# Performance work log

Measured on AMD Instinct MI355X. Metric: run time of the kernel, lower is better.

Reference implementation:

```python
import jax, jax.numpy as jnp
import numpy as np

NA, NF, EA, EF, NG = 200000, 50000, 800000, 200000, 4096
D = 128
BN_EPS = 1e-5

def _bn(x, g, b):
    m = x.mean(axis=0)
    v = x.var(axis=0)
    return g * (x - m) * jax.lax.rsqrt(v + BN_EPS) + b

def _gine(x, src, dst, edge_emb, W1, b1, g1, be1, W2, b2):
    # message = relu(x_src + edge_emb); scatter-add to dst; (1+eps)*x with eps=0
    msg = jax.nn.relu(x[src] + edge_emb)
    agg = jax.ops.segment_sum(msg, dst, num_segments=x.shape[0])
    h = x + agg
    h = jax.nn.relu(_bn(h @ W1 + b1, g1, be1))
    return h @ W2 + b2

def _seg_mean(x, idx, n):
    s = jax.ops.segment_sum(x, idx, num_segments=n)
    c = jax.ops.segment_sum(jnp.ones((x.shape[0],), x.dtype), idx, num_segments=n)
    return s / jnp.maximum(c, 1.0)[:, None]

def setup_inputs() -> dict:
    key = jax.random.key(0)
    ks = jax.random.split(key, 40)
    def nrm(i, shape, scale=0.05):
        return (jax.random.normal(ks[i], shape, dtype=jnp.float32) * scale)
    inp = {
        'atom_x': jax.random.normal(ks[0], (NA, 101), dtype=jnp.float32),
        'fg_x': jax.random.normal(ks[1], (NF, 73), dtype=jnp.float32),
        'atom_edge_attr': jax.random.normal(ks[2], (EA, 11), dtype=jnp.float32),
        'fg_edge_attr': jax.random.normal(ks[3], (EF, 101), dtype=jnp.float32),
        'atom_emb_W': nrm(4, (101, D)), 'atom_emb_b': jnp.zeros((D,), jnp.float32),
        'fg_emb_W': nrm(5, (73, D)), 'fg_emb_b': jnp.zeros((D,), jnp.float32),
        'bond_W': nrm(6, (3, 11, D)), 'bond_b': jnp.zeros((3, D), jnp.float32),
        'ag_W1': nrm(7, (3, D, 2 * D)), 'ag_b1': jnp.zeros((3, 2 * D), jnp.float32),
        'ag_g1': jnp.ones((3, 2 * D), jnp.float32), 'ag_be1': jnp.zeros((3, 2 * D), jnp.float32),
        'ag_W2': nrm(8, (3, 2 * D, D)), 'ag_b2': jnp.zeros((3, D), jnp.float32),
        'abn_g': jnp.ones((3, D), jnp.float32), 'abn_b': jnp.zeros((3, D), jnp.float32),
        'fge_W': nrm(9, (2, 101, D)), 'fge_b': jnp.zeros((2, D), jnp.float32),
        'fg_W1': nrm(10, (2, D, 2 * D)), 'fg_b1': jnp.zeros((2, 2 * D), jnp.float32),
        'fg_g1': jnp.ones((2, 2 * D), jnp.float32), 'fg_be1': jnp.zeros((2, 2 * D), jnp.float32),
        'fg_W2': nrm(11, (2, 2 * D, D)), 'fg_b2': jnp.zeros((2, D), jnp.float32),
        'fbn_g': jnp.ones((2, D), jnp.float32), 'fbn_b': jnp.zeros((2, D), jnp.float32),
        'a2f_W': nrm(12, (D, D)), 'a2f_b': jnp.zeros((D,), jnp.float32),
        'atom_edge_index': jax.random.randint(ks[13], (2, EA), 0, NA, dtype=jnp.int32),
        'fg_edge_index': jax.random.randint(ks[14], (2, EF), 0, NF, dtype=jnp.int32),
        'atom_idx': jax.random.randint(ks[15], (NA,), 0, NA, dtype=jnp.int32),
        'fg_idx': jax.random.randint(ks[16], (NA,), 0, NF, dtype=jnp.int32),
        'fg_batch': jnp.sort(jax.random.randint(ks[17], (NF,), 0, NG, dtype=jnp.int32)),
    }
    return inp

def reference(atom_x, fg_x, atom_edge_attr, fg_edge_attr, atom_emb_W, atom_emb_b, fg_emb_W, fg_emb_b, bond_W, bond_b, ag_W1, ag_b1, ag_g1, ag_be1, ag_W2, ag_b2, abn_g, abn_b, fge_W, fge_b, fg_W1, fg_b1, fg_g1, fg_be1, fg_W2, fg_b2, fbn_g, fbn_b, a2f_W, a2f_b, atom_edge_index, fg_edge_index, atom_idx, fg_idx, fg_batch):
    asrc, adst = atom_edge_index[0], atom_edge_index[1]
    fsrc, fdst = fg_edge_index[0], fg_edge_index[1]
    h = atom_x @ atom_emb_W + atom_emb_b
    for i in range(3):
        eemb = atom_edge_attr @ bond_W[i] + bond_b[i]
        h = _gine(h, asrc, adst, eemb, ag_W1[i], ag_b1[i], ag_g1[i], ag_be1[i], ag_W2[i], ag_b2[i])
        h = _bn(h, abn_g[i], abn_b[i])
        if i != 2:
            h = jax.nn.relu(h)
    a2f = _seg_mean(h[atom_idx], fg_idx, NF) @ a2f_W + a2f_b
    g = fg_x @ fg_emb_W + fg_emb_b + a2f
    for i in range(2):
        eemb = fg_edge_attr @ fge_W[i] + fge_b[i]
        g = _gine(g, fsrc, fdst, eemb, fg_W1[i], fg_b1[i], fg_g1[i], fg_be1[i], fg_W2[i], fg_b2[i])
        g = _bn(g, fbn_g[i], fbn_b[i])
        if i != 1:
            g = jax.nn.relu(g)
    return _seg_mean(g, fg_batch, NG)
```

## Files before the change

### kernel.cpp

```cpp
#include <hip/hip_runtime.h>
#include <cstddef>
#include <cstdint>

#define NA_C 200000
#define NF_C 50000
#define EA_C 800000
#define EF_C 200000
#define NG_C 4096
#define DD 128
#define HH 256
#define SC_CHUNK 2048

typedef unsigned short u16;
typedef unsigned int   u32;
typedef float f32x4 __attribute__((ext_vector_type(4)));
typedef short s16x8 __attribute__((ext_vector_type(8)));

__device__ inline float bf2f(u16 h) { return __uint_as_float(((u32)h) << 16); }
__device__ inline u16 f2bf(float f) {
    u32 u = __float_as_uint(f);
    return (u16)((u + 0x7fffu + ((u >> 16) & 1u)) >> 16);
}
__device__ inline float2 up2(u32 u) {
    return make_float2(__uint_as_float(u << 16), __uint_as_float(u & 0xffff0000u));
}
__device__ inline u32 pk2(float x, float y) { return (u32)f2bf(x) | ((u32)f2bf(y) << 16); }

__global__ __launch_bounds__(256) void gemm_b(
    const u16* __restrict__ A, const u16* __restrict__ Bt,
    const float* __restrict__ bias,
    const float* __restrict__ iscale, const float* __restrict__ ishift,
    const u16* __restrict__ Cadd, u16* __restrict__ C,
    int M, int K, int Ntot,
    float* __restrict__ ssum, float* __restrict__ ssq)
{
    __shared__ u16 As[4 * 128 * 8];
    __shared__ u16 Bs[4 * 128 * 8];
    __shared__ float ls[128], lq[128];
    const int tid  = threadIdx.x;
    const int wave = tid >> 6, lane = tid & 63;
    const int quad = lane >> 4, l15 = lane & 15;
    const int wm = (wave & 1) * 64, wn = (wave >> 1) * 64;
    const int m0 = blockIdx.y * 128, n0 = blockIdx.x * 128;
    const int r     = tid >> 1;
    const int cpair = (tid & 1) * 2;

    f32x4 acc[4][4];
#pragma unroll
    for (int i = 0; i < 4; ++i)
#pragma unroll
        for (int j = 0; j < 4; ++j) acc[i][j] = (f32x4)0.f;

    const int m = m0 + r;
    for (int k0 = 0; k0 < K; k0 += 32) {
#pragma unroll
        for (int j = 0; j < 2; ++j) {
            const int cg = cpair + j;
            uint4 av = make_uint4(0, 0, 0, 0);
            if (m < M) av = *(const uint4*)(A + (size_t)m * K + k0 + cg * 8);
            if (iscale) {
                u32* w = (u32*)&av;
#pragma unroll
                for (int q2 = 0; q2 < 4; ++q2) {
                    int kk = k0 + cg * 8 + q2 * 2;
                    float2 f = up2(w[q2]);
                    f.x = fmaxf(fmaf(f.x, iscale[kk],     ishift[kk]),     0.f);
                    f.y = fmaxf(fmaf(f.y, iscale[kk + 1], ishift[kk + 1]), 0.f);
                    w[q2] = pk2(f.x, f.y);
                }
            }
            *(uint4*)&As[(cg * 128 + r) * 8] = av;
        }
#pragma unroll
        for (int j = 0; j < 2; ++j) {
            const int cg = cpair + j;
            uint4 bv = *(const uint4*)(Bt + (size_t)(n0 + r) * K + k0 + cg * 8);
            *(uint4*)&Bs[(cg * 128 + r) * 8] = bv;
        }
        __syncthreads();

        s16x8 a[4], b[4];
#pragma unroll
        for (int mi = 0; mi < 4; ++mi)
            a[mi] = *(const s16x8*)&As[(quad * 128 + wm + mi * 16 + l15) * 8];
#pragma unroll
        for (int ni = 0; ni < 4; ++ni)
            b[ni] = *(const s16x8*)&Bs[(quad * 128 + wn + ni * 16 + l15) * 8];
#pragma unroll
        for (int mi = 0; mi < 4; ++mi)
#pragma unroll
            for (int ni = 0; ni < 4; ++ni)
                acc[mi][ni] = __builtin_amdgcn_mfma_f32_16x16x32_bf16(
                    a[mi], b[ni], acc[mi][ni], 0, 0, 0);
        __syncthreads();
    }

    if (ssum) {
        if (tid < 128) { ls[tid] = 0.f; lq[tid] = 0.f; }
        __syncthreads();
    }

    float cs[4] = {0.f, 0.f, 0.f, 0.f}, cq[4] = {0.f, 0.f, 0.f, 0.f};
#pragma unroll
    for (int mi = 0; mi < 4; ++mi) {
        int rowb = m0 + wm + mi * 16 + quad * 4;
#pragma unroll
        for (int ni = 0; ni < 4; ++ni) {
            int col = n0 + wn + ni * 16 + l15;
            float bv = bias[col];
#pragma unroll
            for (int rr = 0; rr < 4; ++rr) {
                int row = rowb + rr;
                if (row < M) {
                    float v = acc[mi][ni][rr] + bv;
                    size_t idx = (size_t)row * Ntot + col;
                    if (Cadd) v += bf2f(Cadd[idx]);
                    C[idx] = f2bf(v);
                    cs[ni] += v;
                    cq[ni] = fmaf(v, v, cq[ni]);
                }
            }
        }
    }

    if (ssum) {
#pragma unroll
        for (int ni = 0; ni < 4; ++ni) {
            int lc = wn + ni * 16 + l15;
            atomicAdd(&ls[lc], cs[ni]);
            atomicAdd(&lq[lc], cq[ni]);
        }
        __syncthreads();
        if (tid < 128) {
            atomicAdd(&ssum[n0 + tid], ls[tid]);
            atomicAdd(&ssq[n0 + tid], lq[tid]);
        }
    }
}

static inline void gemm_launch(hipStream_t s, const u16* A, const u16* Bt,
    const float* bias, const float* iscale, const float* ishift,
    const u16* Cadd, u16* C, int M, int K, int Ntot,
    float* ssum = nullptr, float* ssq = nullptr)
{
    dim3 grid(Ntot / 128, (M + 127) / 128);
    gemm_b<<<grid, dim3(256), 0, s>>>(A, Bt, bias, iscale, ishift, Cadd, C,
                                      M, K, Ntot, ssum, ssq);
}

__global__ void cvt_pad(const float* __restrict__ src, u32* __restrict__ dst,
                        int M, int K, int Kp2)
{
    int idx = blockIdx.x * 256 + threadIdx.x;
    if (idx >= M * Kp2) return;
    int row = idx / Kp2, c = (idx - row * Kp2) * 2;
    float a = (c < K)     ? src[(size_t)row * K + c]     : 0.f;
    float b = (c + 1 < K) ? src[(size_t)row * K + c + 1] : 0.f;
    dst[idx] = pk2(a, b);
}

__global__ void cvt_pad_perm(const float* __restrict__ src, const int2* __restrict__ csr2,
                             u32* __restrict__ dst, int M, int K, int Kp2)
{
    int idx = blockIdx.x * 256 + threadIdx.x;
    if (idx >= M * Kp2) return;
    int row = idx / Kp2, c = (idx - row * Kp2) * 2;
    int srow = csr2[row].x;
    float a = (c < K)     ? src[(size_t)srow * K + c]     : 0.f;
    float b = (c + 1 < K) ? src[(size_t)srow * K + c + 1] : 0.f;
    dst[idx] = pk2(a, b);
}

__global__ void perm_attr12_k(const float* __restrict__ attr, const int2* __restrict__ csr2,
                              float* __restrict__ out, int ne)
{
    int idx = blockIdx.x * 256 + threadIdx.x;
    if (idx >= ne * 12) return;
    int e = idx / 12, k = idx - e * 12;
    int eid = csr2[e].x;
    out[idx] = (k < 11) ? attr[(size_t)eid * 11 + k] : 0.f;
}

__global__ void prep_wt(const float* __restrict__ W, u16* __restrict__ Wt,
                        int K, int N, int Kp)
{
    int idx = blockIdx.x * 256 + threadIdx.x;
    if (idx >= N * Kp) return;
    int n = idx / Kp, k = idx - n * Kp;
    Wt[idx] = (k < K) ? f2bf(W[(size_t)k * N + n]) : (u16)0;
}

__global__ void hist_k(const int* __restrict__ idx, int n, int* __restrict__ deg)
{
    int i = blockIdx.x * 256 + threadIdx.x;
    if (i < n) atomicAdd(&deg[idx[i]], 1);
}

__global__ __launch_bounds__(256) void scan_part_k(const int* __restrict__ deg, int n,
                                                   int* __restrict__ bsum)
{
    __shared__ int ts[256];
    const int t = threadIdx.x;
    const int base = blockIdx.x * SC_CHUNK + t * 8;
    int s = 0;
#pragma unroll
    for (int j = 0; j < 8; ++j) { int i = base + j; if (i < n) s += deg[i]; }
    ts[t] = s;
    __syncthreads();
    for (int off = 128; off > 0; off >>= 1) {
        if (t < off) ts[t] += ts[t + off];
        __syncthreads();
    }
    if (t == 0) bsum[blockIdx.x] = ts[0];
}

__global__ __launch_bounds__(256) void scan_top_k(int* __restrict__ bsum, int nb)
{
    __shared__ int ss[256];
    const int t = threadIdx.x;
    int v = (t < nb) ? bsum[t] : 0;
    ss[t] = v;
    __syncthreads();
    for (int off = 1; off < 256; off <<= 1) {
        int u = (t >= off) ? ss[t - off] : 0;
        __syncthreads();
        ss[t] += u;
        __syncthreads();
    }
    if (t < nb) bsum[t] = ss[t] - v;
}

__global__ __launch_bounds__(256) void scan_emit_k(const int* __restrict__ deg, int n,
                                                   const int* __restrict__ bsum,
                                                   int* __restrict__ rowptr)
{
    __shared__ int ts[256];
    const int t = threadIdx.x;
    const int base = blockIdx.x * SC_CHUNK + t * 8;
    int d[8], loc[8], s = 0;
#pragma unroll
    for (int j = 0; j < 8; ++j) {
        int i = base + j;
        d[j] = (i < n) ? deg[i] : 0;
        loc[j] = s;
        s += d[j];
    }
    ts[t] = s;
    __syncthreads();
    for (int off = 1; off < 256; off <<= 1) {
        int u = (t >= off) ? ts[t - off] : 0;
        __syncthreads();
        ts[t] += u;
        __syncthreads();
    }
    const int off0 = bsum[blockIdx.x] + (ts[t] - s);
#pragma unroll
    for (int j = 0; j < 8; ++j) {
        int i = base + j;
        if (i < n) {
            rowptr[i] = off0 + loc[j];
            if (i == n - 1) rowptr[n] = off0 + loc[j] + d[j];
        }
    }
}

static void csr_prefix(hipStream_t s, const int* idx, int ne, int nbkt,
                       int* rowptr, int* cursor, int* bsum)
{
    hipMemsetAsync(cursor, 0, (size_t)nbkt * 4, s);
    hist_k<<<(ne + 255) / 256, 256, 0, s>>>(idx, ne, cursor);
    int nblk = (nbkt + SC_CHUNK - 1) / SC_CHUNK;
    scan_part_k<<<nblk, 256, 0, s>>>(cursor, nbkt, bsum);
    scan_top_k<<<1, 256, 0, s>>>(bsum, nblk);
    scan_emit_k<<<nblk, 256, 0, s>>>(cursor, nbkt, bsum, rowptr);
    hipMemcpyAsync(cursor, rowptr, (size_t)nbkt * 4, hipMemcpyDeviceToDevice, s);
}

__global__ void fill2_k(const int* __restrict__ idx, const int* __restrict__ src,
                        int n, int* __restrict__ cursor, int2* __restrict__ csr2)
{
    int i = blockIdx.x * 256 + threadIdx.x;
    if (i < n) {
        int p = atomicAdd(&cursor[idx[i]], 1);
        csr2[p] = make_int2(i, src[i]);
    }
}

__global__ void fillm_k(const int* __restrict__ idx, const int* __restrict__ map,
                        int n, int* __restrict__ cursor, int* __restrict__ csr)
{
    int i = blockIdx.x * 256 + threadIdx.x;
    if (i < n) {
        int p = atomicAdd(&cursor[idx[i]], 1);
        csr[p] = map ? map[i] : i;
    }
}

__global__ __launch_bounds__(256, 4) void gine_agg_atom_b(
    const u32* __restrict__ x2, const float4* __restrict__ attrp,
    const int2* __restrict__ csr2, const int* __restrict__ rowptr,
    const float* __restrict__ Wm, const float* __restrict__ bm,
    const float* __restrict__ tsc, const float* __restrict__ tsh, int trelu,
    u32* __restrict__ out2, int n)
{
    const int lane = threadIdx.x & 63;
    const int v = blockIdx.x * 4 + (threadIdx.x >> 6);
    if (v >= n) return;
    float wx[11], wy[11];
#pragma unroll
    for (int k = 0; k < 11; ++k) {
        float2 w = *(const float2*)&Wm[k * 128 + 2 * lane];
        wx[k] = w.x; wy[k] = w.y;
    }
    const float2 bb = *(const float2*)&bm[2 * lane];
    float sc0 = 1.f, sc1 = 1.f, sh0 = 0.f, sh1 = 0.f;
    if (tsc) {
        sc0 = tsc[2 * lane]; sc1 = tsc[2 * lane + 1];
        sh0 = tsh[2 * lane]; sh1 = tsh[2 * lane + 1];
    }
    float2 xv = up2(x2[(size_t)v * 64 + lane]);
    xv.x = fmaf(xv.x, sc0, sh0); xv.y = fmaf(xv.y, sc1, sh1);
    if (trelu) { xv.x = fmaxf(xv.x, 0.f); xv.y = fmaxf(xv.y, 0.f); }
    float2 acc = xv;
    const int e0 = rowptr[v], e1 = rowptr[v + 1];
    if (e0 < e1) {
        int2 pc = csr2[e0];
        int2 pn = csr2[(e0 + 1 < e1) ? e0 + 1 : e0];
        float4 a0c = attrp[3 * (size_t)e0];
        float4 a1c = attrp[3 * (size_t)e0 + 1];
        float4 a2c = attrp[3 * (size_t)e0 + 2];
        u32 xc = x2[(size_t)pc.y * 64 + lane];
        for (int e = e0; e < e1; ++e) {
            const int en  = (e + 1 < e1) ? e + 1 : e;
            const int en2 = (e + 2 < e1) ? e + 2 : en;
            int2 p2 = csr2[en2];
            u32 xn = x2[(size_t)pn.y * 64 + lane];
            float4 a0n = attrp[3 * (size_t)en];
            float4 a1n = attrp[3 * (size_t)en + 1];
            float4 a2n = attrp[3 * (size_t)en + 2];
            float ar[12];
            *(float4*)&ar[0] = a0c; *(float4*)&ar[4] = a1c; *(float4*)&ar[8] = a2c;
            float m0 = bb.x, m1 = bb.y;
#pragma unroll
            for (int k = 0; k < 11; ++k) {
                m0 = fmaf(ar[k], wx[k], m0);
                m1 = fmaf(ar[k], wy[k], m1);
            }
            float2 s = up2(xc);
            s.x = fmaf(s.x, sc0, sh0); s.y = fmaf(s.y, sc1, sh1);
            if (trelu) { s.x = fmaxf(s.x, 0.f); s.y = fmaxf(s.y, 0.f); }
            acc.x += fmaxf(s.x + m0, 0.f);
            acc.y += fmaxf(s.y + m1, 0.f);
            pn = p2; xc = xn;
            a0c = a0n; a1c = a1n; a2c = a2n;
        }
    }
    out2[(size_t)v * 64 + lane] = pk2(acc.x, acc.y);
}

__global__ __launch_bounds__(256) void gine_agg_pre_b(
    const u32* __restrict__ x2, const u32* __restrict__ eemb2,
    const int2* __restrict__ csr2, const int* __restrict__ rowptr,
    const float* __restrict__ tsc, const float* __restrict__ tsh, int trelu,
    u32* __restrict__ out2, int n)
{
    const int lane = threadIdx.x & 63;
    const int v = blockIdx.x * 4 + (threadIdx.x >> 6);
    if (v >= n) return;
    float sc0 = 1.f, sc1 = 1.f, sh0 = 0.f, sh1 = 0.f;
    if (tsc) {
        sc0 = tsc[2 * lane]; sc1 = tsc[2 * lane + 1];
        sh0 = tsh[2 * lane]; sh1 = tsh[2 * lane + 1];
    }
    float2 xv = up2(x2[(size_t)v * 64 + lane]);
    xv.x = fmaf(xv.x, sc0, sh0); xv.y = fmaf(xv.y, sc1, sh1);
    if (trelu) { xv.x = fmaxf(xv.x, 0.f); xv.y = fmaxf(xv.y, 0.f); }
    float2 acc = xv;
    const int e0 = rowptr[v], e1 = rowptr[v + 1];
    if (e0 < e1) {
        int2 pc = csr2[e0];
        int2 pn = csr2[(e0 + 1 < e1) ? e0 + 1 : e0];
        u32  xc = x2[(size_t)pc.y * 64 + lane];
        u32  mc = eemb2[(size_t)e0 * 64 + lane];
        for (int e = e0; e < e1; ++e) {
            const int en  = (e + 1 < e1) ? e + 1 : e;
            const int en2 = (e + 2 < e1) ? e + 2 : en;
            int2 p2 = csr2[en2];
            u32  xn = x2[(size_t)pn.y * 64 + lane];
            u32  mn = eemb2[(size_t)en * 64 + lane];
            float2 m = up2(mc);
            float2 s = up2(xc);
            s.x = fmaf(s.x, sc0, sh0); s.y = fmaf(s.y, sc1, sh1);
            if (trelu) { s.x = fmaxf(s.x, 0.f); s.y = fmaxf(s.y, 0.f); }
            acc.x += fmaxf(m.x + s.x, 0.f);
            acc.y += fmaxf(m.y + s.y, 0.f);
            pn = p2; xc = xn; mc = mn;
        }
    }
    out2[(size_t)v * 64 + lane] = pk2(acc.x, acc.y);
}

__global__ __launch_bounds__(256) void seg_mean_b2b(
    const u32* __restrict__ x2, const int* __restrict__ csr,
    const int* __restrict__ rowptr,
    const float* __restrict__ tsc, const float* __restrict__ tsh,
    u32* __restrict__ out2, int n)
{
    const int lane = threadIdx.x & 63;
    const int v = blockIdx.x * 4 + (threadIdx.x >> 6);
    if (v >= n) return;
    const int e0 = rowptr[v], e1 = rowptr[v + 1];
    float2 acc = make_float2(0.f, 0.f);
    if (e0 < e1) {
        int cc = csr[e0];
        int cn = csr[(e0 + 1 < e1) ? e0 + 1 : e0];
        u32 xc = x2[(size_t)cc * 64 + lane];
        for (int e = e0; e < e1; ++e) {
            const int en  = (e + 1 < e1) ? e + 1 : e;
            const int en2 = (e + 2 < e1) ? e + 2 : en;
            int c2 = csr[en2];
            u32 xn = x2[(size_t)cn * 64 + lane];
            float2 s = up2(xc);
            acc.x += s.x; acc.y += s.y;
            cn = c2; xc = xn;
        }
    }
    float inv = 1.f / fmaxf((float)(e1 - e0), 1.f);
    float2 r = make_float2(acc.x * inv, acc.y * inv);
    if (tsc) {
        if (e1 > e0) {
            r.x = fmaf(r.x, tsc[2 * lane],     tsh[2 * lane]);
            r.y = fmaf(r.y, tsc[2 * lane + 1], tsh[2 * lane + 1]);
        } else {
            r.x = 0.f; r.y = 0.f;
        }
    }
    out2[(size_t)v * 64 + lane] = pk2(r.x, r.y);
}

__global__ __launch_bounds__(256) void seg_mean_b2f(
    const u32* __restrict__ x2, const int* __restrict__ csr,
    const int* __restrict__ rowptr,
    const float* __restrict__ tsc, const float* __restrict__ tsh,
    float* __restrict__ out, int n)
{
    const int lane = threadIdx.x & 63;
    const int v = blockIdx.x * 4 + (threadIdx.x >> 6);
    if (v >= n) return;
    const int e0 = rowptr[v], e1 = rowptr[v + 1];
    float2 acc = make_float2(0.f, 0.f);
    if (e0 < e1) {
        int cc = csr[e0];
        int cn = csr[(e0 + 1 < e1) ? e0 + 1 : e0];
        u32 xc = x2[(size_t)cc * 64 + lane];
        for (int e = e0; e < e1; ++e) {
            const int en  = (e + 1 < e1) ? e + 1 : e;
            const int en2 = (e + 2 < e1) ? e + 2 : en;
            int c2 = csr[en2];
            u32 xn = x2[(size_t)cn * 64 + lane];
            float2 s = up2(xc);
            acc.x += s.x; acc.y += s.y;
            cn = c2; xc = xn;
        }
    }
    float inv = 1.f / fmaxf((float)(e1 - e0), 1.f);
    float2 r = make_float2(acc.x * inv, acc.y * inv);
    if (tsc) {
        if (e1 > e0) {
            r.x = fmaf(r.x, tsc[2 * lane],     tsh[2 * lane]);
            r.y = fmaf(r.y, tsc[2 * lane + 1], tsh[2 * lane + 1]);
        } else {
            r.x = 0.f; r.y = 0.f;
        }
    }
    *(float2*)&out[(size_t)v * 128 + lane * 2] = r;
}

__global__ void bn_finalize(const float* __restrict__ sum, const float* __restrict__ sumsq,
                            const float* __restrict__ g, const float* __restrict__ be,
                            float minv, float* __restrict__ sc, float* __restrict__ sh, int N)
{
    int c = threadIdx.x;
    if (c < N) {
        float m = sum[c] * minv;
        float v = fmaxf(sumsq[c] * minv - m * m, 0.f);
        float s = g[c] * rsqrtf(v + 1e-5f);
        sc[c] = s;
        sh[c] = fmaf(-m, s, be[c]);
    }
}

extern "C" void kernel_launch(void* const* d_in, const int* in_sizes, int n_in,
                              void* d_out, int out_size, void* d_ws, size_t ws_size,
                              hipStream_t stream)
{
    const float* atom_x        = (const float*)d_in[0];
    const float* fg_x          = (const float*)d_in[1];
    const float* atom_edge_attr= (const float*)d_in[2];
    const float* fg_edge_attr  = (const float*)d_in[3];
    const float* atom_emb_W    = (const float*)d_in[4];
    const float* atom_emb_b    = (const float*)d_in[5];
    const float* fg_emb_W      = (const float*)d_in[6];
    const float* fg_emb_b      = (const float*)d_in[7];
    const float* bond_W        = (const float*)d_in[8];
    const float* bond_b        = (const float*)d_in[9];
    const float* ag_W1         = (const float*)d_in[10];
    const float* ag_b1         = (const float*)d_in[11];
    const float* ag_g1         = (const float*)d_in[12];
    const float* ag_be1        = (const float*)d_in[13];
    const float* ag_W2         = (const float*)d_in[14];
    const float* ag_b2         = (const float*)d_in[15];
    const float* abn_g         = (const float*)d_in[16];
    const float* abn_b         = (const float*)d_in[17];
    const float* fge_W         = (const float*)d_in[18];
    const float* fge_b         = (const float*)d_in[19];
    const float* fg_W1         = (const float*)d_in[20];
    const float* fg_b1         = (const float*)d_in[21];
    const float* fg_g1         = (const float*)d_in[22];
    const float* fg_be1        = (const float*)d_in[23];
    const float* fg_W2         = (const float*)d_in[24];
    const float* fg_b2         = (const float*)d_in[25];
    const float* fbn_g         = (const float*)d_in[26];
    const float* fbn_b         = (const float*)d_in[27];
    const float* a2f_W         = (const float*)d_in[28];
    const float* a2f_b         = (const float*)d_in[29];
    const int*   aei           = (const int*)d_in[30];
    const int*   fei           = (const int*)d_in[31];
    const int*   atom_idx      = (const int*)d_in[32];
    const int*   fg_idx        = (const int*)d_in[33];
    const int*   fg_batch      = (const int*)d_in[34];
    const int *asrc = aei, *adst = aei + EA_C;
    const int *fsrc = fei, *fdst = fei + EF_C;

    char* base = (char*)d_ws;
    const size_t SZ_H = (size_t)NA_C * DD * 2;
    u16* hA = (u16*)base;
    u16* hB = (u16*)(base + SZ_H);
    u16* TB = (u16*)(base + 2 * SZ_H);
    u16* XB = (u16*)(base + 2 * SZ_H + (size_t)NA_C * HH * 2);
    char* csrb = (char*)XB + SZ_H;
    int*  aR  = (int*)csrb;
    int*  aCu = aR + (NA_C + 2);
    int*  bS  = aCu + NA_C;
    int2* aE2 = (int2*)(bS + 258);
    char* wtb = (char*)(aE2 + EA_C);
    wtb = (char*)(((uintptr_t)wtb + 15) & ~(uintptr_t)15);
    u16* WT_aemb = (u16*)wtb;                 wtb += 128 * 128 * 2;
    u16* WT_aW1  = (u16*)wtb;                 wtb += 3 * 256 * 128 * 2;
    u16* WT_aW2  = (u16*)wtb;                 wtb += 3 * 128 * 256 * 2;
    u16* WT_a2f  = (u16*)wtb;                 wtb += 128 * 128 * 2;
    u16* WT_femb = (u16*)wtb;                 wtb += 128 * 96 * 2;
    u16* WT_fge  = (u16*)wtb;                 wtb += 2 * 128 * 128 * 2;
    u16* WT_fW1  = (u16*)wtb;                 wtb += 2 * 256 * 128 * 2;
    u16* WT_fW2  = (u16*)wtb;                 wtb += 2 * 128 * 256 * 2;
    float* stats = (float*)wtb;               wtb += 10240 * sizeof(float);
    float* S_SUM = stats;
    float* S_SQ  = stats + 2560;
    float* S_SC  = stats + 5120;
    float* S_SH  = stats + 7680;

    {
        int g = (128 * 128 + 255) / 256;
        prep_wt<<<g, 256, 0, stream>>>(atom_emb_W, WT_aemb, 101, 128, 128);
        prep_wt<<<g, 256, 0, stream>>>(a2f_W, WT_a2f, 128, 128, 128);
        for (int i = 0; i < 3; ++i) {
            prep_wt<<<(256 * 128 + 255) / 256, 256, 0, stream>>>(
                ag_W1 + (size_t)i * 128 * 256, WT_aW1 + (size_t)i * 256 * 128, 128, 256, 128);
            prep_wt<<<(128 * 256 + 255) / 256, 256, 0, stream>>>(
                ag_W2 + (size_t)i * 256 * 128, WT_aW2 + (size_t)i * 128 * 256, 256, 128, 256);
        }
        prep_wt<<<(128 * 96 + 255) / 256, 256, 0, stream>>>(fg_emb_W, WT_femb, 73, 128, 96);
        for (int i = 0; i < 2; ++i) {
            prep_wt<<<g, 256, 0, stream>>>(
                fge_W + (size_t)i * 101 * 128, WT_fge + (size_t)i * 128 * 128, 101, 128, 128);
            prep_wt<<<(256 * 128 + 255) / 256, 256, 0, stream>>>(
                fg_W1 + (size_t)i * 128 * 256, WT_fW1 + (size_t)i * 256 * 128, 128, 256, 128);
            prep_wt<<<(128 * 256 + 255) / 256, 256, 0, stream>>>(
                fg_W2 + (size_t)i * 256 * 128, WT_fW2 + (size_t)i * 128 * 256, 256, 128, 256);
        }
    }
    hipMemsetAsync(stats, 0, 5120 * sizeof(float), stream);

    csr_prefix(stream, adst, EA_C, NA_C, aR, aCu, bS);
    fill2_k<<<(EA_C + 255) / 256, 256, 0, stream>>>(adst, asrc, EA_C, aCu, aE2);

    cvt_pad<<<((size_t)NA_C * 64 + 255) / 256, 256, 0, stream>>>(atom_x, (u32*)XB, NA_C, 101, 64);

    gemm_launch(stream, XB, WT_aemb, atom_emb_b, nullptr, nullptr, nullptr, hA, NA_C, 128, 128);

    float* attrP = (float*)XB;
    perm_attr12_k<<<((size_t)EA_C * 12 + 255) / 256, 256, 0, stream>>>(
        atom_edge_attr, aE2, attrP, EA_C);

    u16* hc = hA;
    const float* cur_sc = nullptr;
    const float* cur_sh = nullptr;
    int cur_relu = 0;
    for (int i = 0; i < 3; ++i) {
        u16* hn = (hc == hA) ? hB : hA;
        const int st1 = 2 * i, st2 = 2 * i + 1;
        gine_agg_atom_b<<<(NA_C + 3) / 4, 256, 0, stream>>>(
            (const u32*)hc, (const float4*)attrP, aE2, aR,
            bond_W + (size_t)i * 11 * DD, bond_b + i * DD,
            cur_sc, cur_sh, cur_relu, (u32*)hn, NA_C);
        gemm_launch(stream, hn, WT_aW1 + (size_t)i * 256 * 128,
                    ag_b1 + i * HH, nullptr, nullptr, nullptr, TB, NA_C, 128, HH,
                    S_SUM + st1 * 256, S_SQ + st1 * 256);
        bn_finalize<<<1, HH, 0, stream>>>(S_SUM + st1 * 256, S_SQ + st1 * 256,
                                          ag_g1 + i * HH, ag_be1 + i * HH,
                                          1.f / NA_C, S_SC + st1 * 256, S_SH + st1 * 256, HH);
        gemm_launch(stream, TB, WT_aW2 + (size_t)i * 128 * 256,
                    ag_b2 + i * DD, S_SC + st1 * 256, S_SH + st1 * 256, nullptr, hn,
                    NA_C, 256, 128,
                    S_SUM + st2 * 256, S_SQ + st2 * 256);
        bn_finalize<<<1, DD, 0, stream>>>(S_SUM + st2 * 256, S_SQ + st2 * 256,
                                          abn_g + i * DD, abn_b + i * DD,
                                          1.f / NA_C, S_SC + st2 * 256, S_SH + st2 * 256, DD);
        cur_sc = S_SC + st2 * 256; cur_sh = S_SH + st2 * 256; cur_relu = (i != 2);
        hc = hn;
    }

    {
        int* xE = (int*)aE2;
        csr_prefix(stream, fg_idx, NA_C, NF_C, aR, aCu, bS);
        fillm_k<<<(NA_C + 255) / 256, 256, 0, stream>>>(fg_idx, atom_idx, NA_C, aCu, xE);
        seg_mean_b2b<<<(NF_C + 3) / 4, 256, 0, stream>>>(
            (const u32*)hc, xE, aR, cur_sc, cur_sh, (u32*)hA, NF_C);
    }
    u16* means   = hA;
    u16* a2f_lin = hA + (size_t)NF_C * DD;
    gemm_launch(stream, means, WT_a2f, a2f_b, nullptr, nullptr, nullptr, a2f_lin, NF_C, 128, 128);

    u16* fgx_bf = hA + (size_t)NF_C * DD * 2;
    cvt_pad<<<((size_t)NF_C * 48 + 255) / 256, 256, 0, stream>>>(fg_x, (u32*)fgx_bf, NF_C, 73, 48);
    u16* g = hB;
    gemm_launch(stream, fgx_bf, WT_femb, fg_emb_b, nullptr, nullptr, a2f_lin, g, NF_C, 96, 128);

    csr_prefix(stream, fdst, EF_C, NF_C, aR, aCu, bS);
    fill2_k<<<(EF_C + 255) / 256, 256, 0, stream>>>(fdst, fsrc, EF_C, aCu, aE2);
    cvt_pad_perm<<<((size_t)EF_C * 64 + 255) / 256, 256, 0, stream>>>(
        fg_edge_attr, aE2, (u32*)XB, EF_C, 101, 64);

    u16* eemb = TB;
    u16* gn   = hA + (size_t)NF_C * DD * 2 + (size_t)NF_C * 96;
    u16* gt   = TB + (size_t)EF_C * DD;
    const float* gsc = nullptr;
    const float* gsh = nullptr;
    int grelu = 0;
    for (int i = 0; i < 2; ++i) {
        const int st1 = 6 + 2 * i, st2 = 7 + 2 * i;
        gemm_launch(stream, XB, WT_fge + (size_t)i * 128 * 128,
                    fge_b + i * DD, nullptr, nullptr, nullptr, eemb, EF_C, 128, 128);
        gine_agg_pre_b<<<(NF_C + 3) / 4, 256, 0, stream>>>(
            (const u32*)g, (const u32*)eemb, aE2, aR, gsc, gsh, grelu, (u32*)gn, NF_C);
        gemm_launch(stream, gn, WT_fW1 + (size_t)i * 256 * 128,
                    fg_b1 + i * HH, nullptr, nullptr, nullptr, gt, NF_C, 128, HH,
                    S_SUM + st1 * 256, S_SQ + st1 * 256);
        bn_finalize<<<1, HH, 0, stream>>>(S_SUM + st1 * 256, S_SQ + st1 * 256,
                                          fg_g1 + i * HH, fg_be1 + i * HH,
                                          1.f / NF_C, S_SC + st1 * 256, S_SH + st1 * 256, HH);
        gemm_launch(stream, gt, WT_fW2 + (size_t)i * 128 * 256,
                    fg_b2 + i * DD, S_SC + st1 * 256, S_SH + st1 * 256, nullptr, g,
                    NF_C, 256, 128,
                    S_SUM + st2 * 256, S_SQ + st2 * 256);
        bn_finalize<<<1, DD, 0, stream>>>(S_SUM + st2 * 256, S_SQ + st2 * 256,
                                          fbn_g + i * DD, fbn_b + i * DD,
                                          1.f / NF_C, S_SC + st2 * 256, S_SH + st2 * 256, DD);
        gsc = S_SC + st2 * 256; gsh = S_SH + st2 * 256; grelu = (i != 1);
    }

    {
        int* bR  = (int*)(gt + (size_t)NF_C * HH);
        int* bCu = bR + (NG_C + 1);
        int* bE  = bCu + NG_C;
        csr_prefix(stream, fg_batch, NF_C, NG_C, bR, bCu, bS);
        fillm_k<<<(NF_C + 255) / 256, 256, 0, stream>>>(fg_batch, nullptr, NF_C, bCu, bE);
        seg_mean_b2f<<<(NG_C + 3) / 4, 256, 0, stream>>>(
            (const u32*)g, bE, bR, gsc, gsh, (float*)d_out, NG_C);
    }
}
```

Measured before the change: 2.285 ms.

## Process eight consecutive nodes per wavefront in GINE aggregation kernels

Each wavefront now handles a run of NPW=8 consecutive destination nodes, walking their combined CSR edge range in one software-pipelined loop and flushing the accumulator whenever a node boundary is crossed. This amortizes per-wave setup (bond weight loads, scale/shift loads, pipeline prologue) and keeps the prefetch pipeline full across nodes with few edges. The launch bound occupancy hint is dropped, the grid shrinks eightfold, and the boundary check adds branching inside the inner loop.

```diff
diff --git a/kernel.cpp b/kernel.cpp
--- a/kernel.cpp
+++ b/kernel.cpp
@@ -10,6 +10,7 @@
 #define DD 128
 #define HH 256
 #define SC_CHUNK 2048
+#define NPW 8
 
 typedef unsigned short u16;
 typedef unsigned int   u32;
@@ -296,7 +297,7 @@
     }
 }
 
-__global__ __launch_bounds__(256, 4) void gine_agg_atom_b(
+__global__ __launch_bounds__(256) void gine_agg_atom_b(
     const u32* __restrict__ x2, const float4* __restrict__ attrp,
     const int2* __restrict__ csr2, const int* __restrict__ rowptr,
     const float* __restrict__ Wm, const float* __restrict__ bm,
@@ -304,48 +305,74 @@
     u32* __restrict__ out2, int n)
 {
     const int lane = threadIdx.x & 63;
-    const int v = blockIdx.x * 4 + (threadIdx.x >> 6);
-    if (v >= n) return;
-    float wx[11], wy[11];
-#pragma unroll
-    for (int k = 0; k < 11; ++k) {
-        float2 w = *(const float2*)&Wm[k * 128 + 2 * lane];
-        wx[k] = w.x; wy[k] = w.y;
-    }
+    const int v0 = (blockIdx.x * 4 + (threadIdx.x >> 6)) * NPW;
+    if (v0 >= n) return;
+    const int vend = (v0 + NPW < n) ? v0 + NPW : n;
+
+    const float2 w0 = *(const float2*)&Wm[0 * 128 + 2 * lane];
+    const float2 w1 = *(const float2*)&Wm[1 * 128 + 2 * lane];
+    const float2 w2 = *(const float2*)&Wm[2 * 128 + 2 * lane];
+    const float2 w3 = *(const float2*)&Wm[3 * 128 + 2 * lane];
+    const float2 w4 = *(const float2*)&Wm[4 * 128 + 2 * lane];
+    const float2 w5 = *(const float2*)&Wm[5 * 128 + 2 * lane];
+    const float2 w6 = *(const float2*)&Wm[6 * 128 + 2 * lane];
+    const float2 w7 = *(const float2*)&Wm[7 * 128 + 2 * lane];
+    const float2 w8 = *(const float2*)&Wm[8 * 128 + 2 * lane];
+    const float2 w9 = *(const float2*)&Wm[9 * 128 + 2 * lane];
+    const float2 wa = *(const float2*)&Wm[10 * 128 + 2 * lane];
     const float2 bb = *(const float2*)&bm[2 * lane];
+
     float sc0 = 1.f, sc1 = 1.f, sh0 = 0.f, sh1 = 0.f;
     if (tsc) {
         sc0 = tsc[2 * lane]; sc1 = tsc[2 * lane + 1];
         sh0 = tsh[2 * lane]; sh1 = tsh[2 * lane + 1];
     }
-    float2 xv = up2(x2[(size_t)v * 64 + lane]);
-    xv.x = fmaf(xv.x, sc0, sh0); xv.y = fmaf(xv.y, sc1, sh1);
-    if (trelu) { xv.x = fmaxf(xv.x, 0.f); xv.y = fmaxf(xv.y, 0.f); }
-    float2 acc = xv;
-    const int e0 = rowptr[v], e1 = rowptr[v + 1];
-    if (e0 < e1) {
-        int2 pc = csr2[e0];
-        int2 pn = csr2[(e0 + 1 < e1) ? e0 + 1 : e0];
-        float4 a0c = attrp[3 * (size_t)e0];
-        float4 a1c = attrp[3 * (size_t)e0 + 1];
-        float4 a2c = attrp[3 * (size_t)e0 + 2];
+
+    const int E0 = rowptr[v0], E1 = rowptr[vend];
+    int v  = v0;
+    int nb = rowptr[v0 + 1];
+    u32 xs_n = (v0 + 1 < vend) ? x2[(size_t)(v0 + 1) * 64 + lane] : 0u;
+    float2 acc = up2(x2[(size_t)v0 * 64 + lane]);
+    acc.x = fmaf(acc.x, sc0, sh0); acc.y = fmaf(acc.y, sc1, sh1);
+    if (trelu) { acc.x = fmaxf(acc.x, 0.f); acc.y = fmaxf(acc.y, 0.f); }
+
+    if (E0 < E1) {
+        int2 pc = csr2[E0];
+        int2 pn = csr2[(E0 + 1 < E1) ? E0 + 1 : E0];
+        float4 a0c = attrp[3 * (size_t)E0];
+        float4 a1c = attrp[3 * (size_t)E0 + 1];
+        float4 a2c = attrp[3 * (size_t)E0 + 2];
         u32 xc = x2[(size_t)pc.y * 64 + lane];
-        for (int e = e0; e < e1; ++e) {
-            const int en  = (e + 1 < e1) ? e + 1 : e;
-            const int en2 = (e + 2 < e1) ? e + 2 : en;
+        for (int e = E0; e < E1; ++e) {
+            const int en  = (e + 1 < E1) ? e + 1 : e;
+            const int en2 = (e + 2 < E1) ? e + 2 : en;
             int2 p2 = csr2[en2];
             u32 xn = x2[(size_t)pn.y * 64 + lane];
             float4 a0n = attrp[3 * (size_t)en];
             float4 a1n = attrp[3 * (size_t)en + 1];
             float4 a2n = attrp[3 * (size_t)en + 2];
-            float ar[12];
-            *(float4*)&ar[0] = a0c; *(float4*)&ar[4] = a1c; *(float4*)&ar[8] = a2c;
+            while (e >= nb) {
+                out2[(size_t)v * 64 + lane] = pk2(acc.x, acc.y);
+                ++v;
+                float2 nx = up2(xs_n);
+                nx.x = fmaf(nx.x, sc0, sh0); nx.y = fmaf(nx.y, sc1, sh1);
+                if (trelu) { nx.x = fmaxf(nx.x, 0.f); nx.y = fmaxf(nx.y, 0.f); }
+                acc = nx;
+                xs_n = (v + 1 < vend) ? x2[(size_t)(v + 1) * 64 + lane] : xs_n;
+                nb = rowptr[v + 1];
+            }
             float m0 = bb.x, m1 = bb.y;
-#pragma unroll
-            for (int k = 0; k < 11; ++k) {
-                m0 = fmaf(ar[k], wx[k], m0);
-                m1 = fmaf(ar[k], wy[k], m1);
-            }
+            m0 = fmaf(a0c.x, w0.x, m0); m1 = fmaf(a0c.x, w0.y, m1);
+            m0 = fmaf(a0c.y, w1.x, m0); m1 = fmaf(a0c.y, w1.y, m1);
+            m0 = fmaf(a0c.z, w2.x, m0); m1 = fmaf(a0c.z, w2.y, m1);
+            m0 = fmaf(a0c.w, w3.x, m0); m1 = fmaf(a0c.w, w3.y, m1);
+            m0 = fmaf(a1c.x, w4.x, m0); m1 = fmaf(a1c.x, w4.y, m1);
+            m0 = fmaf(a1c.y, w5.x, m0); m1 = fmaf(a1c.y, w5.y, m1);
+            m0 = fmaf(a1c.z, w6.x, m0); m1 = fmaf(a1c.z, w6.y, m1);
+            m0 = fmaf(a1c.w, w7.x, m0); m1 = fmaf(a1c.w, w7.y, m1);
+            m0 = fmaf(a2c.x, w8.x, m0); m1 = fmaf(a2c.x, w8.y, m1);
+            m0 = fmaf(a2c.y, w9.x, m0); m1 = fmaf(a2c.y, w9.y, m1);
+            m0 = fmaf(a2c.z, wa.x, m0); m1 = fmaf(a2c.z, wa.y, m1);
             float2 s = up2(xc);
             s.x = fmaf(s.x, sc0, sh0); s.y = fmaf(s.y, sc1, sh1);
             if (trelu) { s.x = fmaxf(s.x, 0.f); s.y = fmaxf(s.y, 0.f); }
@@ -355,7 +382,16 @@
             a0c = a0n; a1c = a1n; a2c = a2n;
         }
     }
-    out2[(size_t)v * 64 + lane] = pk2(acc.x, acc.y);
+    for (;;) {
+        out2[(size_t)v * 64 + lane] = pk2(acc.x, acc.y);
+        ++v;
+        if (v >= vend) break;
+        float2 nx = up2(xs_n);
+        nx.x = fmaf(nx.x, sc0, sh0); nx.y = fmaf(nx.y, sc1, sh1);
+        if (trelu) { nx.x = fmaxf(nx.x, 0.f); nx.y = fmaxf(nx.y, 0.f); }
+        acc = nx;
+        xs_n = (v + 1 < vend) ? x2[(size_t)(v + 1) * 64 + lane] : xs_n;
+    }
 }
 
 __global__ __launch_bounds__(256) void gine_agg_pre_b(
@@ -365,29 +401,45 @@
     u32* __restrict__ out2, int n)
 {
     const int lane = threadIdx.x & 63;
-    const int v = blockIdx.x * 4 + (threadIdx.x >> 6);
-    if (v >= n) return;
+    const int v0 = (blockIdx.x * 4 + (threadIdx.x >> 6)) * NPW;
+    if (v0 >= n) return;
+    const int vend = (v0 + NPW < n) ? v0 + NPW : n;
+
     float sc0 = 1.f, sc1 = 1.f, sh0 = 0.f, sh1 = 0.f;
     if (tsc) {
         sc0 = tsc[2 * lane]; sc1 = tsc[2 * lane + 1];
         sh0 = tsh[2 * lane]; sh1 = tsh[2 * lane + 1];
     }
-    float2 xv = up2(x2[(size_t)v * 64 + lane]);
-    xv.x = fmaf(xv.x, sc0, sh0); xv.y = fmaf(xv.y, sc1, sh1);
-    if (trelu) { xv.x = fmaxf(xv.x, 0.f); xv.y = fmaxf(xv.y, 0.f); }
-    float2 acc = xv;
-    const int e0 = rowptr[v], e1 = rowptr[v + 1];
-    if (e0 < e1) {
-        int2 pc = csr2[e0];
-        int2 pn = csr2[(e0 + 1 < e1) ? e0 + 1 : e0];
-        u32  xc = x2[(size_t)pc.y * 64 + lane];
-        u32  mc = eemb2[(size_t)e0 * 64 + lane];
-        for (int e = e0; e < e1; ++e) {
-            const int en  = (e + 1 < e1) ? e + 1 : e;
-            const int en2 = (e + 2 < e1) ? e + 2 : en;
+
+    const int E0 = rowptr[v0], E1 = rowptr[vend];
+    int v  = v0;
+    int nb = rowptr[v0 + 1];
+    u32 xs_n = (v0 + 1 < vend) ? x2[(size_t)(v0 + 1) * 64 + lane] : 0u;
+    float2 acc = up2(x2[(size_t)v0 * 64 + lane]);
+    acc.x = fmaf(acc.x, sc0, sh0); acc.y = fmaf(acc.y, sc1, sh1);
+    if (trelu) { acc.x = fmaxf(acc.x, 0.f); acc.y = fmaxf(acc.y, 0.f); }
+
+    if (E0 < E1) {
+        int2 pc = csr2[E0];
+        int2 pn = csr2[(E0 + 1 < E1) ? E0 + 1 : E0];
+        u32 xc = x2[(size_t)pc.y * 64 + lane];
+        u32 mc = eemb2[(size_t)E0 * 64 + lane];
+        for (int e = E0; e < E1; ++e) {
+            const int en  = (e + 1 < E1) ? e + 1 : e;
+            const int en2 = (e + 2 < E1) ? e + 2 : en;
             int2 p2 = csr2[en2];
-            u32  xn = x2[(size_t)pn.y * 64 + lane];
-            u32  mn = eemb2[(size_t)en * 64 + lane];
+            u32 xn = x2[(size_t)pn.y * 64 + lane];
+            u32 mn = eemb2[(size_t)en * 64 + lane];
+            while (e >= nb) {
+                out2[(size_t)v * 64 + lane] = pk2(acc.x, acc.y);
+                ++v;
+                float2 nx = up2(xs_n);
+                nx.x = fmaf(nx.x, sc0, sh0); nx.y = fmaf(nx.y, sc1, sh1);
+                if (trelu) { nx.x = fmaxf(nx.x, 0.f); nx.y = fmaxf(nx.y, 0.f); }
+                acc = nx;
+                xs_n = (v + 1 < vend) ? x2[(size_t)(v + 1) * 64 + lane] : xs_n;
+                nb = rowptr[v + 1];
+            }
             float2 m = up2(mc);
             float2 s = up2(xc);
             s.x = fmaf(s.x, sc0, sh0); s.y = fmaf(s.y, sc1, sh1);
@@ -397,7 +449,16 @@
             pn = p2; xc = xn; mc = mn;
         }
     }
-    out2[(size_t)v * 64 + lane] = pk2(acc.x, acc.y);
+    for (;;) {
+        out2[(size_t)v * 64 + lane] = pk2(acc.x, acc.y);
+        ++v;
+        if (v >= vend) break;
+        float2 nx = up2(xs_n);
+        nx.x = fmaf(nx.x, sc0, sh0); nx.y = fmaf(nx.y, sc1, sh1);
+        if (trelu) { nx.x = fmaxf(nx.x, 0.f); nx.y = fmaxf(nx.y, 0.f); }
+        acc = nx;
+        xs_n = (v + 1 < vend) ? x2[(size_t)(v + 1) * 64 + lane] : xs_n;
+    }
 }
 
 __global__ __launch_bounds__(256) void seg_mean_b2b(
@@ -592,6 +653,7 @@
     perm_attr12_k<<<((size_t)EA_C * 12 + 255) / 256, 256, 0, stream>>>(
         atom_edge_attr, aE2, attrP, EA_C);
 
+    const int agrid = (NA_C + 4 * NPW - 1) / (4 * NPW);
     u16* hc = hA;
     const float* cur_sc = nullptr;
     const float* cur_sh = nullptr;
@@ -599,7 +661,7 @@
     for (int i = 0; i < 3; ++i) {
         u16* hn = (hc == hA) ? hB : hA;
         const int st1 = 2 * i, st2 = 2 * i + 1;
-        gine_agg_atom_b<<<(NA_C + 3) / 4, 256, 0, stream>>>(
+        gine_agg_atom_b<<<agrid, 256, 0, stream>>>(
             (const u32*)hc, (const float4*)attrP, aE2, aR,
             bond_W + (size_t)i * 11 * DD, bond_b + i * DD,
             cur_sc, cur_sh, cur_relu, (u32*)hn, NA_C);
@@ -641,6 +703,7 @@
     cvt_pad_perm<<<((size_t)EF_C * 64 + 255) / 256, 256, 0, stream>>>(
         fg_edge_attr, aE2, (u32*)XB, EF_C, 101, 64);
 
+    const int fgrid = (NF_C + 4 * NPW - 1) / (4 * NPW);
     u16* eemb = TB;
     u16* gn   = hA + (size_t)NF_C * DD * 2 + (size_t)NF_C * 96;
     u16* gt   = TB + (size_t)EF_C * DD;
@@ -651,7 +714,7 @@
         const int st1 = 6 + 2 * i, st2 = 7 + 2 * i;
         gemm_launch(stream, XB, WT_fge + (size_t)i * 128 * 128,
                     fge_b + i * DD, nullptr, nullptr, nullptr, eemb, EF_C, 128, 128);
-        gine_agg_pre_b<<<(NF_C + 3) / 4, 256, 0, stream>>>(
+        gine_agg_pre_b<<<fgrid, 256, 0, stream>>>(
             (const u32*)g, (const u32*)eemb, aE2, aR, gsc, gsh, grelu, (u32*)gn, NF_C);
         gemm_launch(stream, gn, WT_fW1 + (size_t)i * 256 * 128,
                     fg_b1 + i * HH, nullptr, nullptr, nullptr, gt, NF_C, 128, HH,
```

New measurement: 2.173 ms. 4.9% less time.
